# Performance work log

Hardware: AMD Instinct MI355X
Metric: run time of the kernel (lower is better)

The kernel has to match this reference:

```python
import jax, jax.numpy as jnp
import numpy as np

B, S1, S2, D1, D2, F = 8, 2048, 2048, 512, 512, 256

def setup_inputs() -> dict:
    key = jax.random.key(0)
    ks = jax.random.split(key, 10)
    sc1 = 1.0 / np.sqrt(D1)
    sc2 = 1.0 / np.sqrt(D2)
    scf = 1.0 / np.sqrt(F)
    return {
        "feat1": jax.random.normal(ks[0], (B, S1, D1), jnp.float32),
        "feat2": jax.random.normal(ks[1], (B, S2, D2), jnp.float32),
        "Wq": jax.random.normal(ks[2], (D1, F), jnp.float32) * sc1,
        "bq": jnp.zeros((F,), jnp.float32),
        "Wk": jax.random.normal(ks[3], (D2, F), jnp.float32) * sc2,
        "bk": jnp.zeros((F,), jnp.float32),
        "Wv": jax.random.normal(ks[4], (D2, F), jnp.float32) * sc2,
        "bv": jnp.zeros((F,), jnp.float32),
        "Wfc": jax.random.normal(ks[5], (F, F), jnp.float32) * scf,
        "bfc": jnp.zeros((F,), jnp.float32),
    }

def reference(feat1, feat2, Wq, bq, Wk, bk, Wv, bv, Wfc, bfc):
    Q = jnp.einsum('bsd,df->bsf', feat1, Wq) + bq          # [B,S1,F]
    K = jnp.einsum('btd,df->btf', feat2, Wk) + bk          # [B,S2,F]
    V = jnp.einsum('btd,df->btf', feat2, Wv) + bv          # [B,S2,F]
    scores = jnp.einsum('bsf,btf->bst', Q, K) / jnp.sqrt(jnp.float32(K.shape[-1]))
    attn = jax.nn.softmax(scores, axis=-1)                 # [B,S1,S2]
    attn_out = jnp.einsum('bst,btf->bsf', attn, V)         # [B,S1,F]
    out = jnp.einsum('bsf,fg->bsg', attn_out, Wfc) + bfc   # [B,S1,F]
    return out
```

## Files before the change

kernel.cpp:

```cpp
#include <hip/hip_runtime.h>
#include <hip/hip_bf16.h>

#define B_ 8
#define S1_ 2048
#define S2_ 2048
#define D_ 512
#define F_ 256

typedef __attribute__((ext_vector_type(4))) float f32x4;
typedef __attribute__((ext_vector_type(8))) short s16x8;
typedef __attribute__((ext_vector_type(4))) short s16x4;

__device__ __forceinline__ short f2bf(float x) {
  union { float f; unsigned u; } v; v.f = x;
  unsigned r = v.u + 0x7fffu + ((v.u >> 16) & 1u);
  return (short)(r >> 16);
}

__device__ __forceinline__ int pk2bf(float a, float b) {
  union { __hip_bfloat162 h; int i; } u;
  u.h = __float22bfloat162_rn(make_float2(a, b));
  return u.i;
}

__global__ __launch_bounds__(256) void wtrans_kernel(
    const float* __restrict__ Wq, const float* __restrict__ Wk,
    const float* __restrict__ Wv, const float* __restrict__ Wfc,
    short* __restrict__ Wqt, short* __restrict__ Wkt,
    short* __restrict__ Wvt, short* __restrict__ Wfct) {
  int y = blockIdx.y;
  const float* W; short* Wt; int D;
  if (y == 0)      { W = Wq;  Wt = Wqt;  D = 512; }
  else if (y == 1) { W = Wk;  Wt = Wkt;  D = 512; }
  else if (y == 2) { W = Wv;  Wt = Wvt;  D = 512; }
  else             { W = Wfc; Wt = Wfct; D = 256; }
  int tiles_d = D >> 6;
  int bx = blockIdx.x;
  if (bx >= tiles_d * 4) return;
  int d0 = (bx % tiles_d) * 64, f0 = (bx / tiles_d) * 64;

  __shared__ short Ts[64][68];
  int t = threadIdx.x;
  int r = t >> 2, c16 = (t & 3) * 16;
  {
    const float* src = W + (size_t)(d0 + r) * F_ + f0 + c16;
    f32x4 v0 = *(const f32x4*)(src);
    f32x4 v1 = *(const f32x4*)(src + 4);
    f32x4 v2 = *(const f32x4*)(src + 8);
    f32x4 v3 = *(const f32x4*)(src + 12);
    s16x8 s0, s1;
    ((int*)&s0)[0] = pk2bf(v0[0], v0[1]); ((int*)&s0)[1] = pk2bf(v0[2], v0[3]);
    ((int*)&s0)[2] = pk2bf(v1[0], v1[1]); ((int*)&s0)[3] = pk2bf(v1[2], v1[3]);
    ((int*)&s1)[0] = pk2bf(v2[0], v2[1]); ((int*)&s1)[1] = pk2bf(v2[2], v2[3]);
    ((int*)&s1)[2] = pk2bf(v3[0], v3[1]); ((int*)&s1)[3] = pk2bf(v3[2], v3[3]);
    *(s16x8*)(&Ts[r][c16]) = s0;
    *(s16x8*)(&Ts[r][c16 + 8]) = s1;
  }
  __syncthreads();
  {
    int fr = t >> 2, dc16 = (t & 3) * 16;
    s16x8 o0, o1;
    for (int j = 0; j < 8; ++j) o0[j] = Ts[dc16 + j][fr];
    for (int j = 0; j < 8; ++j) o1[j] = Ts[dc16 + 8 + j][fr];
    short* dst = Wt + (size_t)(f0 + fr) * D + d0 + dc16;
    *(s16x8*)dst = o0;
    *(s16x8*)(dst + 8) = o1;
  }
}

__global__ __launch_bounds__(512, 2) void proj_kernel(
    const float* __restrict__ feat1, const float* __restrict__ feat2,
    const short* __restrict__ Wqt, const short* __restrict__ Wkt,
    const short* __restrict__ Wvt,
    const float* __restrict__ bq, const float* __restrict__ bk,
    const float* __restrict__ bv,
    short* __restrict__ Qw, short* __restrict__ Kw, short* __restrict__ Vtw) {
  const float* A; const short* Wt; const float* bias; short* outp;
  float scale; int trans;
  if (blockIdx.y == 0)      { A = feat1; Wt = Wqt; bias = bq; outp = Qw;  scale = 0.0625f; trans = 0; }
  else if (blockIdx.y == 1) { A = feat2; Wt = Wkt; bias = bk; outp = Kw;  scale = 1.0f;    trans = 0; }
  else                      { A = feat2; Wt = Wvt; bias = bv; outp = Vtw; scale = 1.0f;    trans = 1; }

  __shared__ __align__(16) short As[64][72];
  __shared__ __align__(16) short Ws2[256][72];

  int m0 = blockIdx.x * 64;
  int t = threadIdx.x;
  int w = t >> 6, L = t & 63, rowA = L & 15, quad = L >> 4;
  int wy = w & 1, wx = w >> 1;

  int ar = t >> 3, ac8 = (t & 7) * 8;
  int wr = t >> 1, wc32 = (t & 1) * 32;

  f32x4 av0, av1;
  s16x8 wv[4];
  {
    const float* asrc = A + (size_t)(m0 + ar) * D_ + ac8;
    av0 = *(const f32x4*)(asrc);
    av1 = *(const f32x4*)(asrc + 4);
    const short* wsrc = Wt + (size_t)wr * D_ + wc32;
    for (int j = 0; j < 4; ++j) wv[j] = *(const s16x8*)(wsrc + j * 8);
  }

  f32x4 acc[2][4];
  for (int i = 0; i < 2; ++i)
    for (int j = 0; j < 4; ++j) acc[i][j] = (f32x4){0.f, 0.f, 0.f, 0.f};

  for (int k0 = 0; k0 < D_; k0 += 64) {
    {
      s16x8 s;
      ((int*)&s)[0] = pk2bf(av0[0], av0[1]); ((int*)&s)[1] = pk2bf(av0[2], av0[3]);
      ((int*)&s)[2] = pk2bf(av1[0], av1[1]); ((int*)&s)[3] = pk2bf(av1[2], av1[3]);
      *(s16x8*)(&As[ar][ac8]) = s;
      for (int j = 0; j < 4; ++j) *(s16x8*)(&Ws2[wr][wc32 + j * 8]) = wv[j];
    }
    __syncthreads();
    if (k0 + 64 < D_) {
      const float* asrc = A + (size_t)(m0 + ar) * D_ + k0 + 64 + ac8;
      av0 = *(const f32x4*)(asrc);
      av1 = *(const f32x4*)(asrc + 4);
      const short* wsrc = Wt + (size_t)wr * D_ + k0 + 64 + wc32;
      for (int j = 0; j < 4; ++j) wv[j] = *(const s16x8*)(wsrc + j * 8);
    }
    for (int kt = 0; kt < 2; ++kt) {
      s16x8 a[2];
      for (int mt = 0; mt < 2; ++mt)
        a[mt] = *(const s16x8*)(&As[wy * 32 + mt * 16 + rowA][kt * 32 + quad * 8]);
      for (int nt = 0; nt < 4; ++nt) {
        s16x8 bfr = *(const s16x8*)(&Ws2[wx * 64 + nt * 16 + rowA][kt * 32 + quad * 8]);
        for (int mt = 0; mt < 2; ++mt)
          acc[mt][nt] = __builtin_amdgcn_mfma_f32_16x16x32_bf16(a[mt], bfr, acc[mt][nt], 0, 0, 0);
      }
    }
    __syncthreads();
  }

  if (!trans) {
    float bn[4];
    for (int nt = 0; nt < 4; ++nt) bn[nt] = bias[wx * 64 + nt * 16 + rowA];
    for (int mt = 0; mt < 2; ++mt) {
      int m = m0 + wy * 32 + mt * 16 + quad * 4;
      for (int nt = 0; nt < 4; ++nt) {
        int n = wx * 64 + nt * 16 + rowA;
        for (int r = 0; r < 4; ++r)
          outp[(size_t)(m + r) * F_ + n] = f2bf((acc[mt][nt][r] + bn[nt]) * scale);
      }
    }
  } else {
    int bb = m0 >> 11;
    int tbase = m0 & (S2_ - 1);
    float bn[4];
    for (int nt = 0; nt < 4; ++nt) bn[nt] = bias[wx * 64 + nt * 16 + rowA];
    for (int nt = 0; nt < 4; ++nt) {
      int f = wx * 64 + nt * 16 + rowA;
      for (int mt = 0; mt < 2; ++mt) {
        int tt = tbase + wy * 32 + mt * 16 + quad * 4;
        s16x4 o;
        for (int r = 0; r < 4; ++r) o[r] = f2bf(acc[mt][nt][r] + bn[nt]);
        *(s16x4*)(outp + ((size_t)bb * F_ + f) * S2_ + tt) = o;
      }
    }
  }
}

__global__ __launch_bounds__(512, 2) void flash_kernel(
    const short* __restrict__ Q,
    const short* __restrict__ K,
    const short* __restrict__ Vt,
    const short* __restrict__ Wfct,
    const float* __restrict__ bfc,
    float* __restrict__ out) {
  __shared__ __align__(16) short Ks[2][64][264];
  __shared__ __align__(16) short Vs[2][256][72];
  __shared__ __align__(16) short Ps[2][64][72];

  int b = blockIdx.x >> 5;
  int s0 = (blockIdx.x & 31) * 64;
  int t = threadIdx.x;
  int w = t >> 6, L = t & 63, rowA = L & 15, quad = L >> 4;
  int isS = (w < 4);

  const short* Kb = K + (size_t)b * S2_ * F_;
  const short* Vb = Vt + (size_t)b * F_ * S2_;

  int kr = t >> 5, kc8 = (t & 31) * 8;
  int vr = t >> 3, vc8 = (t & 7) * 8;

  int rs = (w & 1) * 32, cs = ((w >> 1) & 1) * 32;
  int mg = (w - 4) & 1, fg = ((w - 4) >> 1) & 1;

  s16x8 qf[2][8];
  if (isS) {
    const short* Qb = Q + ((size_t)b * S1_ + s0 + rs) * F_;
    for (int mt = 0; mt < 2; ++mt)
      for (int kt = 0; kt < 8; ++kt)
        qf[mt][kt] = *(const s16x8*)(Qb + (size_t)(mt * 16 + rowA) * F_ + kt * 32 + quad * 8);
  }
  f32x4 o[2][8];
  for (int i = 0; i < 2; ++i)
    for (int j = 0; j < 8; ++j) o[i][j] = (f32x4){0.f, 0.f, 0.f, 0.f};
  float l_lane[2][4] = {{0.f,0.f,0.f,0.f},{0.f,0.f,0.f,0.f}};

  s16x8 kpre[4], vpre[4];
  for (int p = 0; p < 4; ++p)
    kpre[p] = *(const s16x8*)(Kb + (size_t)(kr + p * 16) * F_ + kc8);
  for (int p = 0; p < 4; ++p)
    *(s16x8*)(&Ks[0][kr + p * 16][kc8]) = kpre[p];
  for (int p = 0; p < 4; ++p)
    kpre[p] = *(const s16x8*)(Kb + (size_t)(64 + kr + p * 16) * F_ + kc8);
  for (int p = 0; p < 4; ++p)
    vpre[p] = *(const s16x8*)(Vb + (size_t)(vr + p * 64) * S2_ + vc8);

  for (int it = 0; it <= 32; ++it) {
    int cb = it & 1;
    __syncthreads();
    if (it < 32) {
      for (int p = 0; p < 4; ++p)
        *(s16x8*)(&Vs[cb][vr + p * 64][vc8]) = vpre[p];
      if (it < 31) {
        for (int p = 0; p < 4; ++p)
          *(s16x8*)(&Ks[1 - cb][kr + p * 16][kc8]) = kpre[p];
        int n0 = (it + 1) * 64;
        for (int p = 0; p < 4; ++p)
          vpre[p] = *(const s16x8*)(Vb + (size_t)(vr + p * 64) * S2_ + n0 + vc8);
      }
      if (it < 30) {
        int n0 = (it + 2) * 64;
        for (int p = 0; p < 4; ++p)
          kpre[p] = *(const s16x8*)(Kb + (size_t)(n0 + kr + p * 16) * F_ + kc8);
      }
    }
    if (isS) {
      if (it < 32) {
        f32x4 s[2][2];
        for (int i = 0; i < 2; ++i)
          for (int j = 0; j < 2; ++j) s[i][j] = (f32x4){0.f, 0.f, 0.f, 0.f};
        for (int kt = 0; kt < 8; ++kt) {
          s16x8 bf0 = *(const s16x8*)(&Ks[cb][cs + rowA][kt * 32 + quad * 8]);
          s16x8 bf1 = *(const s16x8*)(&Ks[cb][cs + 16 + rowA][kt * 32 + quad * 8]);
          for (int mt = 0; mt < 2; ++mt) {
            s[mt][0] = __builtin_amdgcn_mfma_f32_16x16x32_bf16(qf[mt][kt], bf0, s[mt][0], 0, 0, 0);
            s[mt][1] = __builtin_amdgcn_mfma_f32_16x16x32_bf16(qf[mt][kt], bf1, s[mt][1], 0, 0, 0);
          }
        }
        for (int mt = 0; mt < 2; ++mt)
          for (int nt = 0; nt < 2; ++nt)
            for (int r = 0; r < 4; ++r) {
              float p = __expf(s[mt][nt][r]);
              l_lane[mt][r] += p;
              Ps[cb][rs + mt * 16 + quad * 4 + r][cs + nt * 16 + rowA] = f2bf(p);
            }
      }
    } else {
      if (it > 0) {
        int pb = 1 - cb;
        s16x8 pa[2][2];
        for (int mt = 0; mt < 2; ++mt)
          for (int kt = 0; kt < 2; ++kt)
            pa[mt][kt] = *(const s16x8*)(&Ps[pb][mg * 32 + mt * 16 + rowA][kt * 32 + quad * 8]);
        for (int ft = 0; ft < 8; ++ft)
          for (int kt = 0; kt < 2; ++kt) {
            s16x8 vf = *(const s16x8*)(&Vs[pb][fg * 128 + ft * 16 + rowA][kt * 32 + quad * 8]);
            for (int mt = 0; mt < 2; ++mt)
              o[mt][ft] = __builtin_amdgcn_mfma_f32_16x16x32_bf16(pa[mt][kt], vf, o[mt][ft], 0, 0, 0);
          }
      }
    }
  }

  float* lf = (float*)&Ps[0][0][0];
  short (*Os)[264] = (short(*)[264])&Ks[0][0][0];
  short (*Wg)[132] = (short(*)[132])&Vs[0][0][0];

  if (isS) {
    for (int mt = 0; mt < 2; ++mt)
      for (int r = 0; r < 4; ++r) {
        float x = l_lane[mt][r];
        for (int off = 1; off < 16; off <<= 1)
          x += __shfl_xor(x, off, 64);
        if (rowA == 0)
          lf[((w >> 1) & 1) * 64 + rs + mt * 16 + quad * 4 + r] = x;
      }
  }
  __syncthreads();
  if (!isS) {
    for (int mt = 0; mt < 2; ++mt)
      for (int r = 0; r < 4; ++r) {
        int row = mg * 32 + mt * 16 + quad * 4 + r;
        float inv = 1.0f / (lf[row] + lf[64 + row]);
        for (int ft = 0; ft < 8; ++ft)
          Os[row][fg * 128 + ft * 16 + rowA] = f2bf(o[mt][ft][r] * inv);
      }
  } else {
    const short* src = Wfct + (size_t)t * F_;
    for (int j = 0; j < 16; ++j)
      *(s16x8*)(&Wg[t][j * 8]) = *(const s16x8*)(src + j * 8);
  }
  __syncthreads();

  int fr = w & 3, gh = w >> 2;
  s16x8 af[8];
  for (int kt = 0; kt < 8; ++kt)
    af[kt] = *(const s16x8*)(&Os[fr * 16 + rowA][kt * 32 + quad * 8]);
  f32x4 acc[8];
  for (int i = 0; i < 8; ++i) acc[i] = (f32x4){0.f, 0.f, 0.f, 0.f};

  for (int nt = 0; nt < 8; ++nt) {
    int g = gh * 128 + nt * 16 + rowA;
    for (int kt = 0; kt < 4; ++kt) {
      s16x8 bfr = *(const s16x8*)(&Wg[g][kt * 32 + quad * 8]);
      acc[nt] = __builtin_amdgcn_mfma_f32_16x16x32_bf16(af[kt], bfr, acc[nt], 0, 0, 0);
    }
  }
  __syncthreads();
  {
    int r2 = t >> 1, c2 = (t & 1) * 64;
    const short* src = Wfct + (size_t)r2 * F_ + 128 + c2;
    for (int j = 0; j < 8; ++j)
      *(s16x8*)(&Wg[r2][c2 + j * 8]) = *(const s16x8*)(src + j * 8);
  }
  __syncthreads();
  for (int nt = 0; nt < 8; ++nt) {
    int g = gh * 128 + nt * 16 + rowA;
    for (int kt = 0; kt < 4; ++kt) {
      s16x8 bfr = *(const s16x8*)(&Wg[g][kt * 32 + quad * 8]);
      acc[nt] = __builtin_amdgcn_mfma_f32_16x16x32_bf16(af[4 + kt], bfr, acc[nt], 0, 0, 0);
    }
  }

  float bn[8];
  for (int nt = 0; nt < 8; ++nt) bn[nt] = bfc[gh * 128 + nt * 16 + rowA];
  float* Ob = out + ((size_t)b * S1_ + s0 + fr * 16) * F_;
  for (int nt = 0; nt < 8; ++nt) {
    int g = gh * 128 + nt * 16 + rowA;
    for (int r = 0; r < 4; ++r)
      Ob[(size_t)(quad * 4 + r) * F_ + g] = acc[nt][r] + bn[nt];
  }
}

extern "C" void kernel_launch(void* const* d_in, const int* in_sizes, int n_in,
                              void* d_out, int out_size, void* d_ws, size_t ws_size,
                              hipStream_t stream) {
  const float* feat1 = (const float*)d_in[0];
  const float* feat2 = (const float*)d_in[1];
  const float* Wq  = (const float*)d_in[2];
  const float* bq  = (const float*)d_in[3];
  const float* Wk  = (const float*)d_in[4];
  const float* bk  = (const float*)d_in[5];
  const float* Wv  = (const float*)d_in[6];
  const float* bv  = (const float*)d_in[7];
  const float* Wfc = (const float*)d_in[8];
  const float* bfc = (const float*)d_in[9];
  float* out = (float*)d_out;
  char* ws = (char*)d_ws;

  short* Qw   = (short*)(ws);
  short* Kw   = (short*)(ws + (size_t)(8u  << 20));
  short* Vtw  = (short*)(ws + (size_t)(16u << 20));
  short* Wqt  = (short*)(ws + (size_t)(32u << 20));
  short* Wkt  = Wqt + 256 * 512;
  short* Wvt  = Wkt + 256 * 512;
  short* Wfct = Wvt + 256 * 512;

  wtrans_kernel<<<dim3(32, 4), 256, 0, stream>>>(Wq, Wk, Wv, Wfc, Wqt, Wkt, Wvt, Wfct);
  proj_kernel<<<dim3(256, 3), 512, 0, stream>>>(feat1, feat2, Wqt, Wkt, Wvt,
                                                bq, bk, bv, Qw, Kw, Vtw);
  flash_kernel<<<dim3(256), 512, 0, stream>>>(Qw, Kw, Vtw, Wfct, bfc, out);
}
```

Measured before the change: 209.9 us.

## Split fused output projection out of flash kernel into separate FC GEMM

```diff
diff --git a/kernel.cpp b/kernel.cpp
--- a/kernel.cpp
+++ b/kernel.cpp
@@ -167,15 +167,13 @@
     const short* __restrict__ Q,
     const short* __restrict__ K,
     const short* __restrict__ Vt,
-    const short* __restrict__ Wfct,
-    const float* __restrict__ bfc,
-    float* __restrict__ out) {
+    short* __restrict__ O) {
   __shared__ __align__(16) short Ks[2][64][264];
   __shared__ __align__(16) short Vs[2][256][72];
   __shared__ __align__(16) short Ps[2][64][72];
 
-  int b = blockIdx.x >> 5;
-  int s0 = (blockIdx.x & 31) * 64;
+  int b = blockIdx.x & 7;
+  int s0 = (blockIdx.x >> 3) * 64;
   int t = threadIdx.x;
   int w = t >> 6, L = t & 63, rowA = L & 15, quad = L >> 4;
   int isS = (w < 4);
@@ -268,10 +266,7 @@
     }
   }
 
-  float* lf = (float*)&Ps[0][0][0];
-  short (*Os)[264] = (short(*)[264])&Ks[0][0][0];
-  short (*Wg)[132] = (short(*)[132])&Vs[0][0][0];
-
+  float* lf = (float*)&Ks[0][0][0];
   if (isS) {
     for (int mt = 0; mt < 2; ++mt)
       for (int r = 0; r < 4; ++r) {
@@ -284,57 +279,65 @@
   }
   __syncthreads();
   if (!isS) {
+    short* Ob = O + ((size_t)b * S1_ + s0) * F_;
     for (int mt = 0; mt < 2; ++mt)
       for (int r = 0; r < 4; ++r) {
         int row = mg * 32 + mt * 16 + quad * 4 + r;
         float inv = 1.0f / (lf[row] + lf[64 + row]);
         for (int ft = 0; ft < 8; ++ft)
-          Os[row][fg * 128 + ft * 16 + rowA] = f2bf(o[mt][ft][r] * inv);
-      }
-  } else {
-    const short* src = Wfct + (size_t)t * F_;
-    for (int j = 0; j < 16; ++j)
-      *(s16x8*)(&Wg[t][j * 8]) = *(const s16x8*)(src + j * 8);
-  }
-  __syncthreads();
-
-  int fr = w & 3, gh = w >> 2;
-  s16x8 af[8];
-  for (int kt = 0; kt < 8; ++kt)
-    af[kt] = *(const s16x8*)(&Os[fr * 16 + rowA][kt * 32 + quad * 8]);
-  f32x4 acc[8];
-  for (int i = 0; i < 8; ++i) acc[i] = (f32x4){0.f, 0.f, 0.f, 0.f};
-
-  for (int nt = 0; nt < 8; ++nt) {
-    int g = gh * 128 + nt * 16 + rowA;
-    for (int kt = 0; kt < 4; ++kt) {
-      s16x8 bfr = *(const s16x8*)(&Wg[g][kt * 32 + quad * 8]);
-      acc[nt] = __builtin_amdgcn_mfma_f32_16x16x32_bf16(af[kt], bfr, acc[nt], 0, 0, 0);
-    }
-  }
-  __syncthreads();
-  {
-    int r2 = t >> 1, c2 = (t & 1) * 64;
-    const short* src = Wfct + (size_t)r2 * F_ + 128 + c2;
-    for (int j = 0; j < 8; ++j)
-      *(s16x8*)(&Wg[r2][c2 + j * 8]) = *(const s16x8*)(src + j * 8);
-  }
-  __syncthreads();
-  for (int nt = 0; nt < 8; ++nt) {
-    int g = gh * 128 + nt * 16 + rowA;
-    for (int kt = 0; kt < 4; ++kt) {
-      s16x8 bfr = *(const s16x8*)(&Wg[g][kt * 32 + quad * 8]);
-      acc[nt] = __builtin_amdgcn_mfma_f32_16x16x32_bf16(af[4 + kt], bfr, acc[nt], 0, 0, 0);
-    }
-  }
-
-  float bn[8];
-  for (int nt = 0; nt < 8; ++nt) bn[nt] = bfc[gh * 128 + nt * 16 + rowA];
-  float* Ob = out + ((size_t)b * S1_ + s0 + fr * 16) * F_;
-  for (int nt = 0; nt < 8; ++nt) {
-    int g = gh * 128 + nt * 16 + rowA;
-    for (int r = 0; r < 4; ++r)
-      Ob[(size_t)(quad * 4 + r) * F_ + g] = acc[nt][r] + bn[nt];
+          Ob[(size_t)row * F_ + fg * 128 + ft * 16 + rowA] = f2bf(o[mt][ft][r] * inv);
+      }
+  }
+}
+
+__global__ __launch_bounds__(256) void fc_kernel(
+    const short* __restrict__ AO,
+    const short* __restrict__ Wt,
+    const float* __restrict__ bias,
+    float* __restrict__ out) {
+  __shared__ __align__(16) short As[128][72];
+  __shared__ __align__(16) short Ws[128][72];
+
+  int m0 = blockIdx.x * 128;
+  int n0 = blockIdx.y * 128;
+  int t = threadIdx.x;
+  int w = t >> 6, L = t & 63, rowA = L & 15, quad = L >> 4;
+  int wy = w >> 1, wx = w & 1;
+  int srow = t >> 3, sc8 = (t & 7) * 8;
+
+  f32x4 acc[4][4];
+  for (int i = 0; i < 4; ++i)
+    for (int j = 0; j < 4; ++j) acc[i][j] = (f32x4){0.f, 0.f, 0.f, 0.f};
+
+  for (int k0 = 0; k0 < F_; k0 += 64) {
+    for (int p = 0; p < 4; ++p) {
+      int r = p * 32 + srow;
+      *(s16x8*)(&As[r][sc8]) = *(const s16x8*)(AO + (size_t)(m0 + r) * F_ + k0 + sc8);
+      *(s16x8*)(&Ws[r][sc8]) = *(const s16x8*)(Wt + (size_t)(n0 + r) * F_ + k0 + sc8);
+    }
+    __syncthreads();
+    for (int kt = 0; kt < 2; ++kt) {
+      s16x8 a[4];
+      for (int mt = 0; mt < 4; ++mt)
+        a[mt] = *(const s16x8*)(&As[wy * 64 + mt * 16 + rowA][kt * 32 + quad * 8]);
+      for (int nt = 0; nt < 4; ++nt) {
+        s16x8 bfr = *(const s16x8*)(&Ws[wx * 64 + nt * 16 + rowA][kt * 32 + quad * 8]);
+        for (int mt = 0; mt < 4; ++mt)
+          acc[mt][nt] = __builtin_amdgcn_mfma_f32_16x16x32_bf16(a[mt], bfr, acc[mt][nt], 0, 0, 0);
+      }
+    }
+    __syncthreads();
+  }
+
+  float bn[4];
+  for (int nt = 0; nt < 4; ++nt) bn[nt] = bias[n0 + wx * 64 + nt * 16 + rowA];
+  for (int mt = 0; mt < 4; ++mt) {
+    int m = m0 + wy * 64 + mt * 16 + quad * 4;
+    for (int nt = 0; nt < 4; ++nt) {
+      int n = n0 + wx * 64 + nt * 16 + rowA;
+      for (int r = 0; r < 4; ++r)
+        out[(size_t)(m + r) * F_ + n] = acc[mt][nt][r] + bn[nt];
+    }
   }
 }
 
@@ -357,6 +360,7 @@
   short* Qw   = (short*)(ws);
   short* Kw   = (short*)(ws + (size_t)(8u  << 20));
   short* Vtw  = (short*)(ws + (size_t)(16u << 20));
+  short* AOw  = (short*)(ws + (size_t)(24u << 20));
   short* Wqt  = (short*)(ws + (size_t)(32u << 20));
   short* Wkt  = Wqt + 256 * 512;
   short* Wvt  = Wkt + 256 * 512;
@@ -365,5 +369,6 @@
   wtrans_kernel<<<dim3(32, 4), 256, 0, stream>>>(Wq, Wk, Wv, Wfc, Wqt, Wkt, Wvt, Wfct);
   proj_kernel<<<dim3(256, 3), 512, 0, stream>>>(feat1, feat2, Wqt, Wkt, Wvt,
                                                 bq, bk, bv, Qw, Kw, Vtw);
-  flash_kernel<<<dim3(256), 512, 0, stream>>>(Qw, Kw, Vtw, Wfct, bfc, out);
-}
+  flash_kernel<<<dim3(256), 512, 0, stream>>>(Qw, Kw, Vtw, AOw);
+  fc_kernel<<<dim3(128, 2), 256, 0, stream>>>(AOw, Wfct, bfc, out);
+}
```

New measurement: 205.8 us. About the same (-1.9%).
